# Kernel tuning notes

Hardware: AMD Instinct MI355X
Metric: run time of the kernel (lower is better)

## Reference

```python
import jax, jax.numpy as jnp
import numpy as np

G, N_REAL, C_IN, C_EDGE, H, D, C_EOUT = 4096, 31, 64, 64, 4, 64, 64
N_NODE = N_REAL + 1  # 32, last local node is the supernode


def setup_inputs() -> dict:
    key = jax.random.key(0)
    # per-graph edge template: bidirectional ring over real nodes (consecutive (u,v),(v,u) pairs),
    # then edges (u, supernode)
    u = np.arange(N_REAL)
    v = (u + 1) % N_REAL
    ring_src = np.stack([u, v], 1).reshape(-1)
    ring_dst = np.stack([v, u], 1).reshape(-1)
    ls = np.concatenate([ring_src, np.arange(N_REAL)])
    ld = np.concatenate([ring_dst, np.full(N_REAL, N_REAL)])
    Eg = ls.shape[0]  # 93
    off = np.arange(G) * N_NODE
    edge_index = np.stack([(off[:, None] + ls[None, :]).reshape(-1),
                           (off[:, None] + ld[None, :]).reshape(-1)])
    N = G * N_NODE
    E = G * Eg
    k1, k2, k3, k4, k5 = jax.random.split(key, 5)
    return {
        "x": jax.random.normal(k1, (N, C_IN), jnp.float32),
        "edge_index": jnp.asarray(edge_index, jnp.int32),
        "edge_inform": jax.random.normal(k2, (E, C_EDGE), jnp.float32) * 0.1,
        "batch": jnp.asarray(np.repeat(np.arange(G), N_NODE), jnp.int32),
        "edge_num": jnp.asarray(np.full(G, Eg), jnp.int32),
        "W_lin_l": jax.random.normal(k3, (C_IN + C_EDGE, H * D), jnp.float32) * 0.05,
        "att_l": jax.random.normal(k4, (1, H, D), jnp.float32) * 0.1,
        "bias": jnp.zeros((D,), jnp.float32),
        "W_ec": jax.random.normal(k5, (C_EDGE, C_EOUT), jnp.float32) * 0.1,
        "b_ec": jnp.zeros((C_EOUT,), jnp.float32),
    }


def reference(x, edge_index, edge_inform, batch, edge_num, W_lin_l, att_l, bias, W_ec, b_ec):
    # graph structure is static metadata -> numpy
    ei = np.asarray(edge_index)
    en = np.asarray(edge_num)
    N = x.shape[0]
    G_ = en.shape[0]
    Eg = int(en[0])
    n = N // G_
    src = jnp.asarray(ei[0])
    dst = jnp.asarray(ei[1])
    Hh, Dd = att_l.shape[1], att_l.shape[2]

    # degree counting (the per-edge python loop in the original)
    deg = jnp.zeros((N,), x.dtype).at[dst].add(1.0)

    # GAT-style edge attention + scatter-sum
    h = jnp.concatenate([x[src], edge_inform], axis=1) @ W_lin_l  # [E, H*D]
    h = h.reshape(-1, Hh, Dd)
    alpha = jax.nn.leaky_relu(jnp.sum(h * att_l, axis=-1))  # [E,H], slope 0.01
    amax = jax.ops.segment_max(alpha, dst, num_segments=N)
    ex = jnp.exp(alpha - amax[dst])
    a = ex / (jax.ops.segment_sum(ex, dst, num_segments=N)[dst] + 1e-16)
    xi = jax.ops.segment_sum(h * a[..., None], dst, num_segments=N)  # [N,H,D]
    out = xi.mean(axis=1) + bias

    # per-graph edge aggregation (structure uniform across graphs by construction)
    le = ei.reshape(2, G_, Eg) - (np.arange(G_) * n)[None, :, None]
    l0, l1 = le[0, 0], le[1, 0]  # local template indices, same for every graph
    midx = np.nonzero((l1 != n - 1) & (l0 != l1))[0]  # mask: drop supernode-dst & self-loops
    even = midx[0::2]
    C = edge_inform.shape[1]
    inf_g = edge_inform.reshape(G_, Eg, C)

    mdst = jnp.asarray(l1[midx])
    eisum = jax.vmap(lambda v: jax.ops.segment_sum(v, mdst, num_segments=n - 1))(inf_g[:, midx])  # [G,n-1,C]

    es, ed = l0[even], l1[even]
    deg_g = deg.reshape(G_, n)
    norm = deg_g[:, es] + deg_g[:, ed] - 2.0  # edge_norm; divide by edge_norm - 1
    temp = (eisum[:, es] + eisum[:, ed] - inf_g[:, even]) / (norm - 1.0)[..., None]  # [G,P,C]
    temps2 = jnp.repeat(temp, 2, axis=1)  # each temp appended twice

    l1_all = jnp.asarray(l1)
    cnt = jnp.zeros((n,), x.dtype).at[l1_all].add(1.0)
    esum_all = jax.vmap(lambda v: jax.ops.segment_sum(v, l1_all, num_segments=n))(inf_g)
    emean = esum_all / cnt[None, :, None]  # scatter reduce='mean'

    gather = jnp.concatenate([temps2, emean, emean[:, : n - 1]], axis=1).reshape(-1, C)
    new_edge_inform = jax.nn.leaky_relu(gather @ W_ec + b_ec)
    return out, new_edge_inform
```

## Files before the change

### kernel.cpp

```cpp
#include <hip/hip_runtime.h>
#include <hip/hip_fp16.h>

#define NUM_G 4096
#define OUT2_OFF ((size_t)NUM_G * 32 * 64)

typedef _Float16 half8  __attribute__((ext_vector_type(8)));
typedef _Float16 half4v __attribute__((ext_vector_type(4)));
typedef float    floatx4 __attribute__((ext_vector_type(4)));

__device__ __forceinline__ float lrelu(float v) { return v > 0.f ? v : 0.01f * v; }

__device__ __forceinline__ int swz(int row, int col) {
    return row * 64 + (col ^ ((row & 7) << 3));
}

__global__ void setup_prep(const float* __restrict__ W, const float* __restrict__ att,
                           const float* __restrict__ Wec,
                           _Float16* __restrict__ vp16, _Float16* __restrict__ BT,
                           _Float16* __restrict__ BT2)
{
    const int t = threadIdx.x, b = blockIdx.x;
    if (b < 16) {
        __shared__ _Float16 T[8][256];
        const int kbase = b * 8;
        #pragma unroll
        for (int rr = 0; rr < 8; ++rr)
            T[rr][t] = (_Float16)W[(kbase + rr) * 256 + t];
        __syncthreads();
        const int d = t >> 2, h = t & 3;
        half8 v;
        #pragma unroll
        for (int kk = 0; kk < 8; ++kk) v[kk] = T[kk][h * 64 + d];
        *(half8*)(BT + d * 512 + h * 128 + kbase) = v;
    } else if (b == 16) {
        for (int i = t; i < 1024; i += 256) {
            const int h8 = i >> 6, k = i & 63;
            float acc = 0.f;
            if (h8 < 8) {
                const int h = h8 & 3, ro = (h8 < 4) ? 0 : 64;
                const float4* wr = (const float4*)(W + (ro + k) * 256 + h * 64);
                const float4* ar = (const float4*)(att + h * 64);
                #pragma unroll
                for (int d4 = 0; d4 < 16; ++d4) {
                    float4 wv = wr[d4], av = ar[d4];
                    acc += wv.x * av.x + wv.y * av.y + wv.z * av.z + wv.w * av.w;
                }
            }
            vp16[i] = (_Float16)acc;
        }
    } else {
        __shared__ _Float16 T2[64][65];
        #pragma unroll
        for (int j = 0; j < 16; ++j) {
            const int idx = j * 256 + t;
            T2[idx >> 6][idx & 63] = (_Float16)Wec[idx];
        }
        __syncthreads();
        #pragma unroll
        for (int j = 0; j < 16; ++j) {
            const int idx = j * 256 + t;
            BT2[idx] = T2[idx & 63][idx >> 6];
        }
    }
}

__global__ __launch_bounds__(256, 5) void fused_main(
    const float* __restrict__ x, const float* __restrict__ einf,
    const float* __restrict__ bias, const float* __restrict__ bec,
    const _Float16* __restrict__ vp16, const _Float16* __restrict__ BT,
    const _Float16* __restrict__ BT2,
    float* __restrict__ out, float* __restrict__ out2)
{
    __shared__ __align__(16) _Float16 R[128 * 64];
    __shared__ __align__(16) _Float16 A2[64 * 64];
    __shared__ __align__(16) float    sal[128 * 9];
    __shared__ __align__(16) _Float16 al4h[96 * 4];
    __shared__ __align__(16) _Float16 virt[512];

    const int t = threadIdx.x;
    const int g = blockIdx.x;
    const int lane = t & 63;
    const int w = t >> 6;
    const int m16 = lane & 15, q = lane >> 4;

    {
        const float4* xg4 = (const float4*)(x + (size_t)g * 2048);
        for (int i = t; i < 512; i += 256) {
            float4 v = xg4[i];
            half4v h4 = {(_Float16)v.x, (_Float16)v.y, (_Float16)v.z, (_Float16)v.w};
            *(half4v*)(R + swz(i >> 4, (i & 15) * 4)) = h4;
        }
        const float4* eg4 = (const float4*)(einf + (size_t)g * 5952);
        for (int i = t; i < 1488; i += 256) {
            float4 v = eg4[i];
            half4v h4 = {(_Float16)v.x, (_Float16)v.y, (_Float16)v.z, (_Float16)v.w};
            *(half4v*)(R + swz(32 + (i >> 4), (i & 15) * 4)) = h4;
        }
        if (t < 24) {
            half8 z = {0, 0, 0, 0, 0, 0, 0, 0};
            *(half8*)(R + 125 * 64 + t * 8) = z;
        }
    }
    half8 bF0 = *(const half8*)(vp16 + m16 * 64 + q * 8);
    half8 bF1 = *(const half8*)(vp16 + m16 * 64 + 32 + q * 8);
    __syncthreads();

    #pragma unroll
    for (int j = 0; j < 2; ++j) {
        const int tile = w * 2 + j;
        const int row = tile * 16 + m16;
        half8 aF0 = *(const half8*)(R + swz(row, q * 8));
        half8 aF1 = *(const half8*)(R + swz(row, 32 + q * 8));
        floatx4 s = {0.f, 0.f, 0.f, 0.f};
        s = __builtin_amdgcn_mfma_f32_16x16x32_f16(aF0, bF0, s, 0, 0, 0);
        s = __builtin_amdgcn_mfma_f32_16x16x32_f16(aF1, bF1, s, 0, 0, 0);
        if (m16 < 8) {
            #pragma unroll
            for (int r = 0; r < 4; ++r)
                sal[(tile * 16 + q * 4 + r) * 9 + m16] = s[r];
        }
    }
    __syncthreads();

    if (w == 0) {
        const int i = lane;
        const bool act = (i < 31);
        float av[4], mx[4], wv[4];
        #pragma unroll
        for (int h = 0; h < 4; ++h)
            av[h] = act ? lrelu(sal[i * 9 + h] + sal[(94 + i) * 9 + 4 + h]) : -1e30f;
        #pragma unroll
        for (int h = 0; h < 4; ++h) {
            float m = av[h];
            #pragma unroll
            for (int off = 32; off > 0; off >>= 1)
                m = fmaxf(m, __shfl_xor(m, off, 64));
            mx[h] = m;
        }
        #pragma unroll
        for (int h = 0; h < 4; ++h) {
            float e = act ? __expf(av[h] - mx[h]) : 0.f;
            float s = e;
            #pragma unroll
            for (int off = 32; off > 0; off >>= 1)
                s += __shfl_xor(s, off, 64);
            wv[h] = e / (s + 1e-16f);
        }
        if (act) {
            half4v hv = {(_Float16)wv[0], (_Float16)wv[1], (_Float16)wv[2], (_Float16)wv[3]};
            *(half4v*)(al4h + (62 + i) * 4) = hv;
        }
        asm volatile("s_waitcnt lgkmcnt(0)" ::: "memory");
        __builtin_amdgcn_wave_barrier();
        half8 aV;
        #pragma unroll
        for (int j = 0; j < 8; ++j) {
            const int e = q * 8 + j;
            aV[j] = (m16 < 4 && e < 31) ? al4h[(62 + e) * 4 + m16] : (_Float16)0.f;
        }
        #pragma unroll
        for (int hf = 0; hf < 2; ++hf) {
            const int base = hf ? 94 : 0;
            #pragma unroll
            for (int nt = 0; nt < 4; ++nt) {
                half8 bV;
                #pragma unroll
                for (int j = 0; j < 8; ++j) {
                    const int e = q * 8 + j;
                    bV[j] = (e < 31) ? R[swz(base + e, nt * 16 + m16)] : (_Float16)0.f;
                }
                floatx4 vc = {0.f, 0.f, 0.f, 0.f};
                vc = __builtin_amdgcn_mfma_f32_16x16x32_f16(aV, bV, vc, 0, 0, 0);
                if (q == 0) {
                    #pragma unroll
                    for (int r = 0; r < 4; ++r)
                        virt[r * 128 + hf * 64 + nt * 16 + m16] = (_Float16)vc[r];
                }
            }
        }
    } else if (w == 1) {
        #pragma unroll
        for (int rep = 0; rep < 2; ++rep) {
            const int item = lane * 2 + rep;
            if (item < 124) {
                const int n = item >> 2, h = item & 3;
                const int s1 = (n + 30) % 31, s2 = (n + 1) % 31;
                const int e1 = 2 * s1, e2 = 2 * n + 1;
                const float a1 = lrelu(sal[s1 * 9 + h] + sal[(32 + e1) * 9 + 4 + h]);
                const float a2 = lrelu(sal[s2 * 9 + h] + sal[(32 + e2) * 9 + 4 + h]);
                const float m = fmaxf(a1, a2);
                const float x1 = __expf(a1 - m), x2 = __expf(a2 - m);
                const float inv = 1.f / (x1 + x2 + 1e-16f);
                al4h[e1 * 4 + h] = (_Float16)(x1 * inv);
                al4h[e2 * 4 + h] = (_Float16)(x2 * inv);
            }
        }
    } else {
        for (int idx = t - 128; idx < 992; idx += 128) {
            const int r = idx >> 4, c = (idx & 15) * 4;
            half4v v;
            if (r < 31) {
                const int ra = 2 * ((r + 30) % 31), rb = 2 * r + 1, rc = 2 * ((r + 1) % 31) + 1;
                v = *(const half4v*)(R + swz(32 + ra, c)) + *(const half4v*)(R + swz(32 + rb, c))
                  + *(const half4v*)(R + swz(32 + rc, c));
            } else {
                const int jj = r - 31;
                const int ra = 2 * ((jj + 30) % 31), rb = 2 * jj + 1;
                v = (*(const half4v*)(R + swz(32 + ra, c)) + *(const half4v*)(R + swz(32 + rb, c)))
                    * (_Float16)0.5f;
            }
            *(half4v*)(A2 + swz(r, c)) = v;
        }
        if (t < 192) {
            const int c = t - 128;
            float s = 0.f;
            for (int i = 0; i < 31; ++i) s += (float)R[swz(94 + i, c)];
            A2[swz(62, c)] = (_Float16)(s * (1.f / 31.f));
        } else {
            A2[swz(63, t - 192)] = (_Float16)0.f;
        }
    }
    __syncthreads();

    const int co = w * 16 + m16;
    half8 b2a = *(const half8*)(BT2 + co * 64 + q * 8);
    half8 b2b = *(const half8*)(BT2 + co * 64 + 32 + q * 8);

    {
        const int n1c = (16 + m16 < 31) ? 16 + m16 : 30;
        const int s1_0 = (m16 + 30) % 31, s2_0 = (m16 + 1) % 31;
        const int e1_0 = 2 * s1_0, e2_0 = 2 * m16 + 1;
        const int s1_1 = (n1c + 30) % 31, s2_1 = (n1c + 1) % 31;
        const int e1_1 = 2 * s1_1, e2_1 = 2 * n1c + 1;
        half4v a1_0 = *(const half4v*)(al4h + e1_0 * 4);
        half4v a2_0 = *(const half4v*)(al4h + e2_0 * 4);
        half4v a1_1 = *(const half4v*)(al4h + e1_1 * 4);
        half4v a2_1 = *(const half4v*)(al4h + e2_1 * 4);
        floatx4 acc0 = {0.f, 0.f, 0.f, 0.f}, acc1 = {0.f, 0.f, 0.f, 0.f};
        #pragma unroll
        for (int hf = 0; hf < 2; ++hf) {
            const int rA0 = hf ? 32 + e1_0 : s1_0, rB0 = hf ? 32 + e2_0 : s2_0;
            const int rA1 = hf ? 32 + e1_1 : s1_1, rB1 = hf ? 32 + e2_1 : s2_1;
            #pragma unroll
            for (int kc = 0; kc < 2; ++kc) {
                const int k0 = kc * 32 + q * 8;
                half8 x1 = *(const half8*)(R + swz(rA0, k0));
                half8 x2 = *(const half8*)(R + swz(rB0, k0));
                half8 y1 = *(const half8*)(R + swz(rA1, k0));
                half8 y2 = *(const half8*)(R + swz(rB1, k0));
                #pragma unroll
                for (int h = 0; h < 4; ++h) {
                    half8 b = *(const half8*)(BT + co * 512 + h * 128 + hf * 64 + k0);
                    half8 af0 = x1 * a1_0[h] + x2 * a2_0[h];
                    acc0 = __builtin_amdgcn_mfma_f32_16x16x32_f16(af0, b, acc0, 0, 0, 0);
                    half8 af1 = y1 * a1_1[h] + y2 * a2_1[h];
                    half8 vv = *(const half8*)(virt + h * 128 + hf * 64 + k0);
                    af1 = (m16 == 15) ? vv : af1;
                    acc1 = __builtin_amdgcn_mfma_f32_16x16x32_f16(af1, b, acc1, 0, 0, 0);
                }
            }
        }
        const float bv = bias[co];
        float* og = out + (size_t)g * 2048;
        #pragma unroll
        for (int r = 0; r < 4; ++r) {
            og[(q * 4 + r) * 64 + co]        = 0.25f * acc0[r] + bv;
            og[(16 + q * 4 + r) * 64 + co]   = 0.25f * acc1[r] + bv;
        }
    }

    {
        floatx4 z = {0.f, 0.f, 0.f, 0.f};
        floatx4 acc2[4]; acc2[0] = z; acc2[1] = z; acc2[2] = z; acc2[3] = z;
        #pragma unroll
        for (int kk = 0; kk < 2; ++kk) {
            half8 b = kk ? b2b : b2a;
            #pragma unroll
            for (int mt = 0; mt < 4; ++mt) {
                half8 a = *(const half8*)(A2 + swz(mt * 16 + m16, kk * 32 + q * 8));
                acc2[mt] = __builtin_amdgcn_mfma_f32_16x16x32_f16(a, b, acc2[mt], 0, 0, 0);
            }
        }
        const float bv2 = bec[co];
        float* o2 = out2 + (size_t)g * 8000;
        #pragma unroll
        for (int mt = 0; mt < 4; ++mt) {
            #pragma unroll
            for (int r = 0; r < 4; ++r) {
                const int row = mt * 16 + q * 4 + r;
                if (row >= 63) continue;
                const float v = lrelu(acc2[mt][r] + bv2);
                if (row < 31) {
                    o2[(2 * row) * 64 + co]     = v;
                    o2[(2 * row + 1) * 64 + co] = v;
                } else if (row < 62) {
                    o2[(62 + row - 31) * 64 + co] = v;
                    o2[(94 + row - 31) * 64 + co] = v;
                } else {
                    o2[93 * 64 + co] = v;
                }
            }
        }
    }
}

extern "C" void kernel_launch(void* const* d_in, const int* in_sizes, int n_in,
                              void* d_out, int out_size, void* d_ws, size_t ws_size,
                              hipStream_t stream) {
    const float* x    = (const float*)d_in[0];
    const float* einf = (const float*)d_in[2];
    const float* W    = (const float*)d_in[5];
    const float* att  = (const float*)d_in[6];
    const float* bias = (const float*)d_in[7];
    const float* Wec  = (const float*)d_in[8];
    const float* bec  = (const float*)d_in[9];
    float* out  = (float*)d_out;
    float* out2 = out + OUT2_OFF;

    _Float16* vp16 = (_Float16*)d_ws;
    _Float16* BT   = (_Float16*)((char*)d_ws + 2048);
    _Float16* BT2  = (_Float16*)((char*)d_ws + 2048 + 65536);

    setup_prep<<<18, 256, 0, stream>>>(W, att, Wec, vp16, BT, BT2);
    fused_main<<<NUM_G, 256, 0, stream>>>(x, einf, bias, bec, vp16, BT, BT2, out, out2);
}
```

Before: 322.9 us.

## Process two graphs per block to reuse weight fragments and rebalance waves

Each workgroup now handles two graphs, so the LDS buffers are doubled and the grid is halved. Per-graph attention and softmax work is split so that waves 0-1 each take one graph's supernode path and waves 2-3 each take one graph's ring softmax and edge aggregation. The main MFMA loops reuse each loaded weight fragment across both graphs. The cost is twice the LDS per block, lower occupancy (launch bounds reduced from 5 to 2), and half as many blocks to hide the memory latency of what is a bandwidth-bound kernel.

```diff
diff --git a/kernel.cpp b/kernel.cpp
--- a/kernel.cpp
+++ b/kernel.cpp
@@ -64,41 +64,42 @@
     }
 }
 
-__global__ __launch_bounds__(256, 5) void fused_main(
+__global__ __launch_bounds__(256, 2) void fused_main(
     const float* __restrict__ x, const float* __restrict__ einf,
     const float* __restrict__ bias, const float* __restrict__ bec,
     const _Float16* __restrict__ vp16, const _Float16* __restrict__ BT,
     const _Float16* __restrict__ BT2,
     float* __restrict__ out, float* __restrict__ out2)
 {
-    __shared__ __align__(16) _Float16 R[128 * 64];
-    __shared__ __align__(16) _Float16 A2[64 * 64];
-    __shared__ __align__(16) float    sal[128 * 9];
-    __shared__ __align__(16) _Float16 al4h[96 * 4];
-    __shared__ __align__(16) _Float16 virt[512];
+    __shared__ __align__(16) _Float16 R[2][128 * 64];
+    __shared__ __align__(16) _Float16 A2[2][64 * 64];
+    __shared__ __align__(16) float    sal[2][128 * 9];
+    __shared__ __align__(16) _Float16 al4h[2][96 * 4];
+    __shared__ __align__(16) _Float16 virt[2][512];
 
     const int t = threadIdx.x;
-    const int g = blockIdx.x;
+    const int g0 = blockIdx.x * 2;
     const int lane = t & 63;
     const int w = t >> 6;
     const int m16 = lane & 15, q = lane >> 4;
 
-    {
-        const float4* xg4 = (const float4*)(x + (size_t)g * 2048);
+    #pragma unroll
+    for (int gi = 0; gi < 2; ++gi) {
+        const float4* xg4 = (const float4*)(x + (size_t)(g0 + gi) * 2048);
         for (int i = t; i < 512; i += 256) {
             float4 v = xg4[i];
             half4v h4 = {(_Float16)v.x, (_Float16)v.y, (_Float16)v.z, (_Float16)v.w};
-            *(half4v*)(R + swz(i >> 4, (i & 15) * 4)) = h4;
-        }
-        const float4* eg4 = (const float4*)(einf + (size_t)g * 5952);
+            *(half4v*)(R[gi] + swz(i >> 4, (i & 15) * 4)) = h4;
+        }
+        const float4* eg4 = (const float4*)(einf + (size_t)(g0 + gi) * 5952);
         for (int i = t; i < 1488; i += 256) {
             float4 v = eg4[i];
             half4v h4 = {(_Float16)v.x, (_Float16)v.y, (_Float16)v.z, (_Float16)v.w};
-            *(half4v*)(R + swz(32 + (i >> 4), (i & 15) * 4)) = h4;
+            *(half4v*)(R[gi] + swz(32 + (i >> 4), (i & 15) * 4)) = h4;
         }
         if (t < 24) {
             half8 z = {0, 0, 0, 0, 0, 0, 0, 0};
-            *(half8*)(R + 125 * 64 + t * 8) = z;
+            *(half8*)(R[gi] + 125 * 64 + t * 8) = z;
         }
     }
     half8 bF0 = *(const half8*)(vp16 + m16 * 64 + q * 8);
@@ -106,29 +107,33 @@
     __syncthreads();
 
     #pragma unroll
-    for (int j = 0; j < 2; ++j) {
-        const int tile = w * 2 + j;
-        const int row = tile * 16 + m16;
-        half8 aF0 = *(const half8*)(R + swz(row, q * 8));
-        half8 aF1 = *(const half8*)(R + swz(row, 32 + q * 8));
-        floatx4 s = {0.f, 0.f, 0.f, 0.f};
-        s = __builtin_amdgcn_mfma_f32_16x16x32_f16(aF0, bF0, s, 0, 0, 0);
-        s = __builtin_amdgcn_mfma_f32_16x16x32_f16(aF1, bF1, s, 0, 0, 0);
-        if (m16 < 8) {
-            #pragma unroll
-            for (int r = 0; r < 4; ++r)
-                sal[(tile * 16 + q * 4 + r) * 9 + m16] = s[r];
+    for (int gi = 0; gi < 2; ++gi) {
+        #pragma unroll
+        for (int j = 0; j < 2; ++j) {
+            const int tile = w * 2 + j;
+            const int row = tile * 16 + m16;
+            half8 aF0 = *(const half8*)(R[gi] + swz(row, q * 8));
+            half8 aF1 = *(const half8*)(R[gi] + swz(row, 32 + q * 8));
+            floatx4 s = {0.f, 0.f, 0.f, 0.f};
+            s = __builtin_amdgcn_mfma_f32_16x16x32_f16(aF0, bF0, s, 0, 0, 0);
+            s = __builtin_amdgcn_mfma_f32_16x16x32_f16(aF1, bF1, s, 0, 0, 0);
+            if (m16 < 8) {
+                #pragma unroll
+                for (int r = 0; r < 4; ++r)
+                    sal[gi][(tile * 16 + q * 4 + r) * 9 + m16] = s[r];
+            }
         }
     }
     __syncthreads();
 
-    if (w == 0) {
+    if (w < 2) {
+        const int gi = w;
         const int i = lane;
         const bool act = (i < 31);
         float av[4], mx[4], wv[4];
         #pragma unroll
         for (int h = 0; h < 4; ++h)
-            av[h] = act ? lrelu(sal[i * 9 + h] + sal[(94 + i) * 9 + 4 + h]) : -1e30f;
+            av[h] = act ? lrelu(sal[gi][i * 9 + h] + sal[gi][(94 + i) * 9 + 4 + h]) : -1e30f;
         #pragma unroll
         for (int h = 0; h < 4; ++h) {
             float m = av[h];
@@ -148,7 +153,7 @@
         }
         if (act) {
             half4v hv = {(_Float16)wv[0], (_Float16)wv[1], (_Float16)wv[2], (_Float16)wv[3]};
-            *(half4v*)(al4h + (62 + i) * 4) = hv;
+            *(half4v*)(al4h[gi] + (62 + i) * 4) = hv;
         }
         asm volatile("s_waitcnt lgkmcnt(0)" ::: "memory");
         __builtin_amdgcn_wave_barrier();
@@ -156,7 +161,7 @@
         #pragma unroll
         for (int j = 0; j < 8; ++j) {
             const int e = q * 8 + j;
-            aV[j] = (m16 < 4 && e < 31) ? al4h[(62 + e) * 4 + m16] : (_Float16)0.f;
+            aV[j] = (m16 < 4 && e < 31) ? al4h[gi][(62 + e) * 4 + m16] : (_Float16)0.f;
         }
         #pragma unroll
         for (int hf = 0; hf < 2; ++hf) {
@@ -167,18 +172,19 @@
                 #pragma unroll
                 for (int j = 0; j < 8; ++j) {
                     const int e = q * 8 + j;
-                    bV[j] = (e < 31) ? R[swz(base + e, nt * 16 + m16)] : (_Float16)0.f;
+                    bV[j] = (e < 31) ? R[gi][swz(base + e, nt * 16 + m16)] : (_Float16)0.f;
                 }
                 floatx4 vc = {0.f, 0.f, 0.f, 0.f};
                 vc = __builtin_amdgcn_mfma_f32_16x16x32_f16(aV, bV, vc, 0, 0, 0);
                 if (q == 0) {
                     #pragma unroll
                     for (int r = 0; r < 4; ++r)
-                        virt[r * 128 + hf * 64 + nt * 16 + m16] = (_Float16)vc[r];
-                }
-            }
-        }
-    } else if (w == 1) {
+                        virt[gi][r * 128 + hf * 64 + nt * 16 + m16] = (_Float16)vc[r];
+                }
+            }
+        }
+    } else {
+        const int gi = w - 2;
         #pragma unroll
         for (int rep = 0; rep < 2; ++rep) {
             const int item = lane * 2 + rep;
@@ -186,38 +192,36 @@
                 const int n = item >> 2, h = item & 3;
                 const int s1 = (n + 30) % 31, s2 = (n + 1) % 31;
                 const int e1 = 2 * s1, e2 = 2 * n + 1;
-                const float a1 = lrelu(sal[s1 * 9 + h] + sal[(32 + e1) * 9 + 4 + h]);
-                const float a2 = lrelu(sal[s2 * 9 + h] + sal[(32 + e2) * 9 + 4 + h]);
+                const float a1 = lrelu(sal[gi][s1 * 9 + h] + sal[gi][(32 + e1) * 9 + 4 + h]);
+                const float a2 = lrelu(sal[gi][s2 * 9 + h] + sal[gi][(32 + e2) * 9 + 4 + h]);
                 const float m = fmaxf(a1, a2);
                 const float x1 = __expf(a1 - m), x2 = __expf(a2 - m);
                 const float inv = 1.f / (x1 + x2 + 1e-16f);
-                al4h[e1 * 4 + h] = (_Float16)(x1 * inv);
-                al4h[e2 * 4 + h] = (_Float16)(x2 * inv);
-            }
-        }
-    } else {
-        for (int idx = t - 128; idx < 992; idx += 128) {
+                al4h[gi][e1 * 4 + h] = (_Float16)(x1 * inv);
+                al4h[gi][e2 * 4 + h] = (_Float16)(x2 * inv);
+            }
+        }
+        for (int idx = lane; idx < 992; idx += 64) {
             const int r = idx >> 4, c = (idx & 15) * 4;
             half4v v;
             if (r < 31) {
                 const int ra = 2 * ((r + 30) % 31), rb = 2 * r + 1, rc = 2 * ((r + 1) % 31) + 1;
-                v = *(const half4v*)(R + swz(32 + ra, c)) + *(const half4v*)(R + swz(32 + rb, c))
-                  + *(const half4v*)(R + swz(32 + rc, c));
+                v = *(const half4v*)(R[gi] + swz(32 + ra, c)) + *(const half4v*)(R[gi] + swz(32 + rb, c))
+                  + *(const half4v*)(R[gi] + swz(32 + rc, c));
             } else {
                 const int jj = r - 31;
                 const int ra = 2 * ((jj + 30) % 31), rb = 2 * jj + 1;
-                v = (*(const half4v*)(R + swz(32 + ra, c)) + *(const half4v*)(R + swz(32 + rb, c)))
+                v = (*(const half4v*)(R[gi] + swz(32 + ra, c)) + *(const half4v*)(R[gi] + swz(32 + rb, c)))
                     * (_Float16)0.5f;
             }
-            *(half4v*)(A2 + swz(r, c)) = v;
-        }
-        if (t < 192) {
-            const int c = t - 128;
+            *(half4v*)(A2[gi] + swz(r, c)) = v;
+        }
+        {
+            const int c = lane;
             float s = 0.f;
-            for (int i = 0; i < 31; ++i) s += (float)R[swz(94 + i, c)];
-            A2[swz(62, c)] = (_Float16)(s * (1.f / 31.f));
-        } else {
-            A2[swz(63, t - 192)] = (_Float16)0.f;
+            for (int i = 0; i < 31; ++i) s += (float)R[gi][swz(94 + i, c)];
+            A2[gi][swz(62, c)] = (_Float16)(s * (1.f / 31.f));
+            A2[gi][swz(63, c)] = (_Float16)0.f;
         }
     }
     __syncthreads();
@@ -232,11 +236,16 @@
         const int e1_0 = 2 * s1_0, e2_0 = 2 * m16 + 1;
         const int s1_1 = (n1c + 30) % 31, s2_1 = (n1c + 1) % 31;
         const int e1_1 = 2 * s1_1, e2_1 = 2 * n1c + 1;
-        half4v a1_0 = *(const half4v*)(al4h + e1_0 * 4);
-        half4v a2_0 = *(const half4v*)(al4h + e2_0 * 4);
-        half4v a1_1 = *(const half4v*)(al4h + e1_1 * 4);
-        half4v a2_1 = *(const half4v*)(al4h + e2_1 * 4);
-        floatx4 acc0 = {0.f, 0.f, 0.f, 0.f}, acc1 = {0.f, 0.f, 0.f, 0.f};
+        half4v a1_0[2], a2_0[2], a1_1[2], a2_1[2];
+        #pragma unroll
+        for (int gi = 0; gi < 2; ++gi) {
+            a1_0[gi] = *(const half4v*)(al4h[gi] + e1_0 * 4);
+            a2_0[gi] = *(const half4v*)(al4h[gi] + e2_0 * 4);
+            a1_1[gi] = *(const half4v*)(al4h[gi] + e1_1 * 4);
+            a2_1[gi] = *(const half4v*)(al4h[gi] + e2_1 * 4);
+        }
+        floatx4 z = {0.f, 0.f, 0.f, 0.f};
+        floatx4 acc0[2] = {z, z}, acc1[2] = {z, z};
         #pragma unroll
         for (int hf = 0; hf < 2; ++hf) {
             const int rA0 = hf ? 32 + e1_0 : s1_0, rB0 = hf ? 32 + e2_0 : s2_0;
@@ -244,60 +253,80 @@
             #pragma unroll
             for (int kc = 0; kc < 2; ++kc) {
                 const int k0 = kc * 32 + q * 8;
-                half8 x1 = *(const half8*)(R + swz(rA0, k0));
-                half8 x2 = *(const half8*)(R + swz(rB0, k0));
-                half8 y1 = *(const half8*)(R + swz(rA1, k0));
-                half8 y2 = *(const half8*)(R + swz(rB1, k0));
+                half8 x1[2], x2[2], y1[2], y2[2];
+                #pragma unroll
+                for (int gi = 0; gi < 2; ++gi) {
+                    x1[gi] = *(const half8*)(R[gi] + swz(rA0, k0));
+                    x2[gi] = *(const half8*)(R[gi] + swz(rB0, k0));
+                    y1[gi] = *(const half8*)(R[gi] + swz(rA1, k0));
+                    y2[gi] = *(const half8*)(R[gi] + swz(rB1, k0));
+                }
                 #pragma unroll
                 for (int h = 0; h < 4; ++h) {
                     half8 b = *(const half8*)(BT + co * 512 + h * 128 + hf * 64 + k0);
-                    half8 af0 = x1 * a1_0[h] + x2 * a2_0[h];
-                    acc0 = __builtin_amdgcn_mfma_f32_16x16x32_f16(af0, b, acc0, 0, 0, 0);
-                    half8 af1 = y1 * a1_1[h] + y2 * a2_1[h];
-                    half8 vv = *(const half8*)(virt + h * 128 + hf * 64 + k0);
-                    af1 = (m16 == 15) ? vv : af1;
-                    acc1 = __builtin_amdgcn_mfma_f32_16x16x32_f16(af1, b, acc1, 0, 0, 0);
+                    #pragma unroll
+                    for (int gi = 0; gi < 2; ++gi) {
+                        half8 af0 = x1[gi] * a1_0[gi][h] + x2[gi] * a2_0[gi][h];
+                        acc0[gi] = __builtin_amdgcn_mfma_f32_16x16x32_f16(af0, b, acc0[gi], 0, 0, 0);
+                        half8 af1 = y1[gi] * a1_1[gi][h] + y2[gi] * a2_1[gi][h];
+                        half8 vv = *(const half8*)(virt[gi] + h * 128 + hf * 64 + k0);
+                        af1 = (m16 == 15) ? vv : af1;
+                        acc1[gi] = __builtin_amdgcn_mfma_f32_16x16x32_f16(af1, b, acc1[gi], 0, 0, 0);
+                    }
                 }
             }
         }
         const float bv = bias[co];
-        float* og = out + (size_t)g * 2048;
-        #pragma unroll
-        for (int r = 0; r < 4; ++r) {
-            og[(q * 4 + r) * 64 + co]        = 0.25f * acc0[r] + bv;
-            og[(16 + q * 4 + r) * 64 + co]   = 0.25f * acc1[r] + bv;
+        #pragma unroll
+        for (int gi = 0; gi < 2; ++gi) {
+            float* og = out + (size_t)(g0 + gi) * 2048;
+            #pragma unroll
+            for (int r = 0; r < 4; ++r) {
+                og[(q * 4 + r) * 64 + co]        = 0.25f * acc0[gi][r] + bv;
+                og[(16 + q * 4 + r) * 64 + co]   = 0.25f * acc1[gi][r] + bv;
+            }
         }
     }
 
     {
         floatx4 z = {0.f, 0.f, 0.f, 0.f};
-        floatx4 acc2[4]; acc2[0] = z; acc2[1] = z; acc2[2] = z; acc2[3] = z;
+        floatx4 acc2[2][4];
+        #pragma unroll
+        for (int gi = 0; gi < 2; ++gi)
+            #pragma unroll
+            for (int mt = 0; mt < 4; ++mt) acc2[gi][mt] = z;
         #pragma unroll
         for (int kk = 0; kk < 2; ++kk) {
             half8 b = kk ? b2b : b2a;
             #pragma unroll
+            for (int gi = 0; gi < 2; ++gi) {
+                #pragma unroll
+                for (int mt = 0; mt < 4; ++mt) {
+                    half8 a = *(const half8*)(A2[gi] + swz(mt * 16 + m16, kk * 32 + q * 8));
+                    acc2[gi][mt] = __builtin_amdgcn_mfma_f32_16x16x32_f16(a, b, acc2[gi][mt], 0, 0, 0);
+                }
+            }
+        }
+        const float bv2 = bec[co];
+        #pragma unroll
+        for (int gi = 0; gi < 2; ++gi) {
+            float* o2 = out2 + (size_t)(g0 + gi) * 8000;
+            #pragma unroll
             for (int mt = 0; mt < 4; ++mt) {
-                half8 a = *(const half8*)(A2 + swz(mt * 16 + m16, kk * 32 + q * 8));
-                acc2[mt] = __builtin_amdgcn_mfma_f32_16x16x32_f16(a, b, acc2[mt], 0, 0, 0);
-            }
-        }
-        const float bv2 = bec[co];
-        float* o2 = out2 + (size_t)g * 8000;
-        #pragma unroll
-        for (int mt = 0; mt < 4; ++mt) {
-            #pragma unroll
-            for (int r = 0; r < 4; ++r) {
-                const int row = mt * 16 + q * 4 + r;
-                if (row >= 63) continue;
-                const float v = lrelu(acc2[mt][r] + bv2);
-                if (row < 31) {
-                    o2[(2 * row) * 64 + co]     = v;
-                    o2[(2 * row + 1) * 64 + co] = v;
-                } else if (row < 62) {
-                    o2[(62 + row - 31) * 64 + co] = v;
-                    o2[(94 + row - 31) * 64 + co] = v;
-                } else {
-                    o2[93 * 64 + co] = v;
+                #pragma unroll
+                for (int r = 0; r < 4; ++r) {
+                    const int row = mt * 16 + q * 4 + r;
+                    if (row >= 63) continue;
+                    const float v = lrelu(acc2[gi][mt][r] + bv2);
+                    if (row < 31) {
+                        o2[(2 * row) * 64 + co]     = v;
+                        o2[(2 * row + 1) * 64 + co] = v;
+                    } else if (row < 62) {
+                        o2[(62 + row - 31) * 64 + co] = v;
+                        o2[(94 + row - 31) * 64 + co] = v;
+                    } else {
+                        o2[93 * 64 + co] = v;
+                    }
                 }
             }
         }
@@ -322,5 +351,5 @@
     _Float16* BT2  = (_Float16*)((char*)d_ws + 2048 + 65536);
 
     setup_prep<<<18, 256, 0, stream>>>(W, att, Wec, vp16, BT, BT2);
-    fused_main<<<NUM_G, 256, 0, stream>>>(x, einf, bias, bec, vp16, BT, BT2, out, out2);
+    fused_main<<<NUM_G / 2, 256, 0, stream>>>(x, einf, bias, bec, vp16, BT, BT2, out, out2);
 }
```

Result: no change. 326.3 us (+1.1%).
